# Performance work log

Hardware: AMD Instinct MI355X
Metric: run time of the kernel (lower is better)

The kernel has to match this reference:

```python
import jax, jax.numpy as jnp
import numpy as np

NUM_HEADS = 12
HEAD_SIZE = 64
HIDDEN = NUM_HEADS * HEAD_SIZE  # 768
ONE_SIDED_WINDOW = 256          # attention_window 512 // 2
NEG = -10000.0


def setup_inputs() -> dict:
    key = jax.random.key(0)
    ks = jax.random.split(key, 16)
    B, W, E, H = 1, 2048, 128, HIDDEN
    std = 0.02
    def lin(kw, kb):
        return (jax.random.normal(kw, (H, H), jnp.float32) * std,
                jax.random.normal(kb, (H,), jnp.float32) * std)
    q_w, q_b = lin(ks[0], ks[1])
    k_w, k_b = lin(ks[2], ks[3])
    v_w, v_b = lin(ks[4], ks[5])
    w2e_w, w2e_b = lin(ks[6], ks[7])
    e2w_w, e2w_b = lin(ks[8], ks[9])
    e2e_w, e2e_b = lin(ks[10], ks[11])
    return {
        "word_hidden_states": jax.random.normal(ks[12], (B, W, H), jnp.float32),
        "entity_hidden_states": jax.random.normal(ks[13], (B, E, H), jnp.float32),
        "attention_mask": jnp.zeros((B, 1, 1, W + E), jnp.float32),
        "q_w": q_w, "q_b": q_b, "k_w": k_w, "k_b": k_b, "v_w": v_w, "v_b": v_b,
        "w2e_w": w2e_w, "w2e_b": w2e_b, "e2w_w": e2w_w, "e2w_b": e2w_b,
        "e2e_w": e2e_w, "e2e_b": e2e_b,
    }


def reference(word_hidden_states, entity_hidden_states, attention_mask,
              q_w, q_b, k_w, k_b, v_w, v_b,
              w2e_w, w2e_b, e2w_w, e2w_b, e2e_w, e2e_b):
    B, W, H = word_hidden_states.shape
    E = entity_hidden_states.shape[1]
    S = W + E

    def heads(x):  # [B, L, H] -> [B, nh, L, hd]
        return x.reshape(B, -1, NUM_HEADS, HEAD_SIZE).transpose(0, 2, 1, 3)

    concat = jnp.concatenate([word_hidden_states, entity_hidden_states], axis=1)
    k = heads(concat @ k_w + k_b)          # [B, nh, S, hd]
    v = heads(concat @ v_w + v_b)
    q_w2w = heads(word_hidden_states @ q_w + q_b)
    q_w2e = heads(word_hidden_states @ w2e_w + w2e_b)
    q_e2w = heads(entity_hidden_states @ e2w_w + e2w_b)
    q_e2e = heads(entity_hidden_states @ e2e_w + e2e_b)

    k_word, k_ent = k[:, :, :W], k[:, :, W:]

    # --- w2w: Longformer sliding-window QK^T, then _conversion to a dense
    # [B, nh, W, W] matrix with out-of-band entries set to -10000. ---
    w2w = jnp.einsum('bhid,bhjd->bhij', q_w2w, k_word)  # [B, nh, W, W]
    idx = jnp.arange(W)
    in_band = jnp.abs(idx[:, None] - idx[None, :]) <= ONE_SIDED_WINDOW  # [W, W]
    # diagonal mask: float_mask[j] (-10000 where attention_mask != 0) added
    # within the band (broadcast over heads / query positions)
    mask_words = attention_mask[:, 0, 0, :W]                # [B, W]
    float_mask = jnp.where(mask_words != 0.0, NEG, 0.0)     # [B, W]
    w2w = w2w + float_mask[:, None, None, :]
    # _conversion: out-of-band -> -10000; also exact zeros -> -10000 (source quirk)
    w2w = jnp.where(in_band[None, None] & (w2w != 0.0), w2w, NEG)

    # --- entity-aware dense blocks ---
    w2e = jnp.einsum('bhid,bhjd->bhij', q_w2e, k_ent)    # [B, nh, W, E]
    e2w = jnp.einsum('bhid,bhjd->bhij', q_e2w, k_word)   # [B, nh, E, W]
    e2e = jnp.einsum('bhid,bhjd->bhij', q_e2e, k_ent)    # [B, nh, E, E]

    word_scores = jnp.concatenate([w2w, w2e], axis=3)    # [B, nh, W, S]
    ent_scores = jnp.concatenate([e2w, e2e], axis=3)     # [B, nh, E, S]
    scores = jnp.concatenate([word_scores, ent_scores], axis=2)  # [B, nh, S, S]

    scores = scores / jnp.sqrt(jnp.float32(HEAD_SIZE)) + attention_mask
    probs = jax.nn.softmax(scores, axis=-1)

    ctx = jnp.einsum('bhij,bhjd->bhid', probs, v)        # [B, nh, S, hd]
    ctx = ctx.transpose(0, 2, 1, 3).reshape(B, S, H)
    return ctx[:, :W, :], ctx[:, W:, :]
```

## Files before the change

kernel.cpp:

```cpp
#include <hip/hip_runtime.h>

typedef __bf16 bf16x8 __attribute__((ext_vector_type(8)));
typedef unsigned short u16x8 __attribute__((ext_vector_type(8)));
typedef u16x8 u16x8_a __attribute__((may_alias));
typedef unsigned int u32x4 __attribute__((ext_vector_type(4)));
typedef u32x4 u32x4_a __attribute__((may_alias));
typedef float f32x4 __attribute__((ext_vector_type(4)));

#define LOG2E 1.4426950408889634f
#define NEGV  -10000.0f

__device__ __forceinline__ float bf2f(unsigned short u){
  union{unsigned int i; float f;} x; x.i = ((unsigned int)u)<<16; return x.f;
}
__device__ __forceinline__ unsigned short f2bf(float f){
  union{float f; unsigned int i;} x; x.f=f;
  unsigned int i = x.i;
  return (unsigned short)((i + 0x7FFFu + ((i>>16)&1u)) >> 16);
}
__device__ __forceinline__ u16x8 cvt8(float4 a, float4 b){
  u16x8 r;
  r[0]=f2bf(a.x); r[1]=f2bf(a.y); r[2]=f2bf(a.z); r[3]=f2bf(a.w);
  r[4]=f2bf(b.x); r[5]=f2bf(b.y); r[6]=f2bf(b.z); r[7]=f2bf(b.w);
  return r;
}
__device__ __forceinline__ bf16x8 ldb(const unsigned short* p){
  return __builtin_bit_cast(bf16x8, *(const u16x8_a*)p);
}

__global__ __launch_bounds__(256) void transpose6(
    const float* __restrict__ w0, const float* __restrict__ w1,
    const float* __restrict__ w2, const float* __restrict__ w3,
    const float* __restrict__ w4, const float* __restrict__ w5,
    unsigned short* __restrict__ outT)
{
  const float* src;
  switch (blockIdx.z){
    case 0: src = w0; break; case 1: src = w1; break; case 2: src = w2; break;
    case 3: src = w3; break; case 4: src = w4; break; default: src = w5; break;
  }
  unsigned short* dst = outT + (size_t)blockIdx.z * 589824;
  __shared__ float tile[32][33];
  int tx = threadIdx.x, ty = threadIdx.y;
  int x0 = blockIdx.x*32, y0 = blockIdx.y*32;
  #pragma unroll
  for (int i=0;i<32;i+=8) tile[ty+i][tx] = src[(size_t)(y0+ty+i)*768 + x0+tx];
  __syncthreads();
  #pragma unroll
  for (int i=0;i<32;i+=8) dst[(size_t)(x0+ty+i)*768 + y0+tx] = f2bf(tile[tx][ty+i]);
}

__global__ __launch_bounds__(256) void transpose_v(
    const unsigned short* __restrict__ Vb, unsigned short* __restrict__ VbT)
{
  __shared__ unsigned short t[32][33];
  int tx = threadIdx.x, ty = threadIdx.y;
  int x0 = blockIdx.x*32;
  int y0 = blockIdx.y*32;
  #pragma unroll
  for (int i=0;i<32;i+=8) t[ty+i][tx] = Vb[(size_t)(x0+ty+i)*768 + y0+tx];
  __syncthreads();
  #pragma unroll
  for (int i=0;i<32;i+=8) VbT[(size_t)(y0+ty+i)*2176 + x0+tx] = t[tx][ty+i];
}

__global__ __launch_bounds__(256) void gemm_proj(
    const float* __restrict__ word, const float* __restrict__ ent,
    const unsigned short* __restrict__ wT,
    const float* __restrict__ bK, const float* __restrict__ bV,
    const float* __restrict__ bQ, const float* __restrict__ bWE,
    const float* __restrict__ bEW, const float* __restrict__ bEE,
    unsigned short* __restrict__ oK, unsigned short* __restrict__ oV,
    unsigned short* __restrict__ oQ, unsigned short* __restrict__ oWE,
    unsigned short* __restrict__ oEW, unsigned short* __restrict__ oEE)
{
  int mt = blockIdx.x, ntile = blockIdx.y;
  int g, mg;
  if      (mt < 17){ g=0; mg=mt;    }
  else if (mt < 34){ g=1; mg=mt-17; }
  else if (mt < 50){ g=2; mg=mt-34; }
  else if (mt < 66){ g=3; mg=mt-50; }
  else if (mt < 67){ g=4; mg=0;     }
  else             { g=5; mg=0;     }
  int m0 = mg*128;
  const float* A;
  if (g<=1)      A = (mg<16) ? (word + (size_t)m0*768) : ent;
  else if (g<=3) A = word + (size_t)m0*768;
  else           A = ent;
  const unsigned short* B = wT + (size_t)g*589824;
  const float* bias; unsigned short* out;
  switch (g){
    case 0: bias=bK;  out=oK;  break;
    case 1: bias=bV;  out=oV;  break;
    case 2: bias=bQ;  out=oQ;  break;
    case 3: bias=bWE; out=oWE; break;
    case 4: bias=bEW; out=oEW; break;
    default:bias=bEE; out=oEE; break;
  }
  out += (size_t)m0*768;
  int n0 = ntile*128;

  __shared__ __align__(16) unsigned short a_s[128*32];
  __shared__ __align__(16) unsigned short b_s[128*32];

  int tid  = threadIdx.x;
  int w    = tid>>6, lane = tid&63, quad = lane>>4, lr = lane&15;
  int wm   = (w&1)*64, wn = (w>>1)*64;

  f32x4 acc[4][4];
  #pragma unroll
  for (int i=0;i<4;i++) for (int j=0;j<4;j++) for (int r=0;r<4;r++) acc[i][j][r]=0.f;

  int ar = tid>>1;
  int ak = (tid&1)*16;
  const float* Arow = A + (size_t)ar*768 + ak;
  const unsigned short* Brow = B + (size_t)(n0+ar)*768 + ak;

  for (int k0=0; k0<768; k0+=32){
    float4 af0 = *(const float4*)(Arow + k0);
    float4 af1 = *(const float4*)(Arow + k0 + 4);
    float4 af2 = *(const float4*)(Arow + k0 + 8);
    float4 af3 = *(const float4*)(Arow + k0 + 12);
    u16x8 av0 = cvt8(af0, af1);
    u16x8 av1 = cvt8(af2, af3);
    u16x8 bv0 = *(const u16x8_a*)(Brow + k0);
    u16x8 bv1 = *(const u16x8_a*)(Brow + k0 + 8);
    __syncthreads();
    *(u16x8_a*)(a_s + ar*32 + ak)     = av0;
    *(u16x8_a*)(a_s + ar*32 + ak + 8) = av1;
    *(u16x8_a*)(b_s + ar*32 + ak)     = bv0;
    *(u16x8_a*)(b_s + ar*32 + ak + 8) = bv1;
    __syncthreads();
    bf16x8 af[4], bfr[4];
    #pragma unroll
    for (int i=0;i<4;i++) af[i]  = ldb(a_s + (wm+i*16+lr)*32 + quad*8);
    #pragma unroll
    for (int i=0;i<4;i++) bfr[i] = ldb(b_s + (wn+i*16+lr)*32 + quad*8);
    #pragma unroll
    for (int i=0;i<4;i++)
      #pragma unroll
      for (int j=0;j<4;j++)
        acc[i][j] = __builtin_amdgcn_mfma_f32_16x16x32_bf16(af[i], bfr[j], acc[i][j], 0,0,0);
  }
  #pragma unroll
  for (int j=0;j<4;j++){
    int col = n0 + wn + j*16 + lr;
    float bb = bias[col];
    #pragma unroll
    for (int i=0;i<4;i++){
      int rowb = wm + i*16 + quad*4;
      #pragma unroll
      for (int r=0;r<4;r++)
        out[(size_t)(rowb+r)*768 + col] = f2bf(acc[i][j][r] + bb);
    }
  }
}

__global__ __launch_bounds__(256) void attn_split(
  const unsigned short* __restrict__ Kb,  const unsigned short* __restrict__ VbT,
  const unsigned short* __restrict__ Qw,  const unsigned short* __restrict__ Qwe,
  const unsigned short* __restrict__ Qew, const unsigned short* __restrict__ Qee,
  const float* __restrict__ am,
  float* __restrict__ outw, float* __restrict__ oute)
{
  int bx = blockIdx.x, h = blockIdx.y;
  int tid = threadIdx.x, w = tid>>6, lane = tid&63, quad = lane>>4, lr = lane&15;
  bool isword = bx < 64;
  int qrb, kh, nsplit;
  const unsigned short *Qa, *Qb;
  float* outp;
  if (isword){ qrb = bx*32 + (w>>1)*16; kh = w&1; nsplit = 2; Qa=Qw;  Qb=Qwe; outp=outw; }
  else       { qrb = (bx-64)*16;        kh = w;   nsplit = 4; Qa=Qew; Qb=Qee; outp=oute; }

  __shared__ __align__(16) unsigned int p32[4][16*24];
  __shared__ float mrg[4][64][24];

  const unsigned short* qr = Qa + (size_t)(qrb+lr)*768 + h*64 + quad*8;
  bf16x8 qa0 = ldb(qr), qa1 = ldb(qr + 32);
  qr = Qb + (size_t)(qrb+lr)*768 + h*64 + quad*8;
  bf16x8 qb0 = ldb(qr), qb1 = ldb(qr + 32);

  float m_r[4], l_r[4];
  f32x4 o[4];
  #pragma unroll
  for (int r=0;r<4;r++){ m_r[r] = -1e30f; l_r[r] = 0.f; }
  #pragma unroll
  for (int n2=0;n2<4;n2++) for (int r=0;r<4;r++) o[n2][r] = 0.f;

  int lo, nw;
  if (isword){
    lo = qrb - 256; if (lo < 0) lo = 0; lo &= ~31;
    int hi = qrb + 272; if (hi > 2048) hi = 2048; hi = (hi + 31) & ~31;
    nw = (hi - lo) >> 5;
  } else { lo = 0; nw = 64; }
  int nc = nw + 4;

  for (int c = kh; c < nc; c += nsplit){
    bool entp = c >= nw;
    int j0 = entp ? (2048 + (c-nw)*32) : (lo + c*32);

    const unsigned short* kp = Kb + (size_t)(j0+lr)*768 + h*64 + quad*8;
    bf16x8 k00 = ldb(kp),          k01 = ldb(kp + 32);
    bf16x8 k10 = ldb(kp + 16*768), k11 = ldb(kp + 16*768 + 32);
    const unsigned short* vp = VbT + (size_t)(h*64 + lr)*2176 + j0 + quad*8;
    bf16x8 v0 = ldb(vp), v1 = ldb(vp + 16*2176), v2 = ldb(vp + 32*2176), v3 = ldb(vp + 48*2176);

    bf16x8 qf0 = entp ? qb0 : qa0;
    bf16x8 qf1 = entp ? qb1 : qa1;
    f32x4 s[2];
    {
      f32x4 z0 = {0.f,0.f,0.f,0.f}, z1 = {0.f,0.f,0.f,0.f};
      z0 = __builtin_amdgcn_mfma_f32_16x16x32_bf16(qf0, k00, z0, 0,0,0);
      z0 = __builtin_amdgcn_mfma_f32_16x16x32_bf16(qf1, k01, z0, 0,0,0);
      z1 = __builtin_amdgcn_mfma_f32_16x16x32_bf16(qf0, k10, z1, 0,0,0);
      z1 = __builtin_amdgcn_mfma_f32_16x16x32_bf16(qf1, k11, z1, 0,0,0);
      s[0] = z0; s[1] = z1;
    }

    float sc[2][4];
    bool wband = isword && !entp;
    #pragma unroll
    for (int t=0;t<2;t++){
      int j = j0 + t*16 + lr;
      float amj  = am[j];
      float addl = amj * LOG2E;
      #pragma unroll
      for (int r=0;r<4;r++){
        float sv = s[t][r];
        if (wband){
          sv += (amj != 0.f) ? NEGV : 0.f;
          int i = qrb + quad*4 + r;
          bool ok = ((unsigned)(i - j + 256) <= 512u) && (sv != 0.f);
          sv = ok ? sv : NEGV;
        }
        sc[t][r] = sv * (LOG2E*0.125f) + addl;
      }
    }

    #pragma unroll
    for (int r=0;r<4;r++){
      float mx = fmaxf(sc[0][r], sc[1][r]);
      mx = fmaxf(mx, __shfl_xor(mx, 1));
      mx = fmaxf(mx, __shfl_xor(mx, 2));
      mx = fmaxf(mx, __shfl_xor(mx, 4));
      mx = fmaxf(mx, __shfl_xor(mx, 8));
      float mn = fmaxf(m_r[r], mx);
      float alpha = exp2f(m_r[r] - mn);
      m_r[r] = mn;
      float p0 = exp2f(sc[0][r]-mn), p1 = exp2f(sc[1][r]-mn);
      unsigned short pb0 = f2bf(p0), pb1 = f2bf(p1);
      float rs = bf2f(pb0) + bf2f(pb1);
      rs += __shfl_xor(rs,1); rs += __shfl_xor(rs,2);
      rs += __shfl_xor(rs,4); rs += __shfl_xor(rs,8);
      l_r[r] = l_r[r]*alpha + rs;
      p32[w][(quad*4+r)*24 + lr] = (unsigned int)pb0 | ((unsigned int)pb1 << 16);
      #pragma unroll
      for (int n2=0;n2<4;n2++) o[n2][r] *= alpha;
    }

    const unsigned int* pbp = &p32[w][lr*24 + (quad&1)*8];
    u32x4 ra = *(const u32x4_a*)pbp;
    u32x4 rb = *(const u32x4_a*)(pbp + 4);
    unsigned int pf32[4];
    if (quad < 2){
      pf32[0] = (ra[0]&0xFFFFu) | (ra[1]<<16);
      pf32[1] = (ra[2]&0xFFFFu) | (ra[3]<<16);
      pf32[2] = (rb[0]&0xFFFFu) | (rb[1]<<16);
      pf32[3] = (rb[2]&0xFFFFu) | (rb[3]<<16);
    } else {
      pf32[0] = (ra[0]>>16) | (ra[1]&0xFFFF0000u);
      pf32[1] = (ra[2]>>16) | (ra[3]&0xFFFF0000u);
      pf32[2] = (rb[0]>>16) | (rb[1]&0xFFFF0000u);
      pf32[3] = (rb[2]>>16) | (rb[3]&0xFFFF0000u);
    }
    u32x4 pfv = {pf32[0], pf32[1], pf32[2], pf32[3]};
    bf16x8 pf = __builtin_bit_cast(bf16x8, pfv);

    o[0] = __builtin_amdgcn_mfma_f32_16x16x32_bf16(pf, v0, o[0], 0,0,0);
    o[1] = __builtin_amdgcn_mfma_f32_16x16x32_bf16(pf, v1, o[1], 0,0,0);
    o[2] = __builtin_amdgcn_mfma_f32_16x16x32_bf16(pf, v2, o[2], 0,0,0);
    o[3] = __builtin_amdgcn_mfma_f32_16x16x32_bf16(pf, v3, o[3], 0,0,0);
  }

  {
    float* my = &mrg[w][lane][0];
    #pragma unroll
    for (int r=0;r<4;r++){ my[r] = m_r[r]; my[4+r] = l_r[r]; }
    #pragma unroll
    for (int n2=0;n2<4;n2++)
      #pragma unroll
      for (int r=0;r<4;r++) my[8+n2*4+r] = o[n2][r];
  }
  __syncthreads();
  if (kh == 0){
    for (int p=1; p<nsplit; p++){
      const float* pr = &mrg[w+p][lane][0];
      #pragma unroll
      for (int r=0;r<4;r++){
        float m2 = pr[r], l2 = pr[4+r];
        float M  = fmaxf(m_r[r], m2);
        float e1 = exp2f(m_r[r]-M), e2 = exp2f(m2-M);
        m_r[r] = M;
        l_r[r] = l_r[r]*e1 + l2*e2;
        #pragma unroll
        for (int n2=0;n2<4;n2++)
          o[n2][r] = o[n2][r]*e1 + pr[8+n2*4+r]*e2;
      }
    }
    #pragma unroll
    for (int n2=0;n2<4;n2++)
      #pragma unroll
      for (int r=0;r<4;r++){
        int row = qrb + quad*4 + r;
        outp[(size_t)row*768 + h*64 + n2*16 + lr] = o[n2][r] / l_r[r];
      }
  }
}

extern "C" void kernel_launch(void* const* d_in, const int* in_sizes, int n_in,
                              void* d_out, int out_size, void* d_ws, size_t ws_size,
                              hipStream_t stream) {
  const float* word  = (const float*)d_in[0];
  const float* ent   = (const float*)d_in[1];
  const float* am    = (const float*)d_in[2];
  const float* q_w   = (const float*)d_in[3];
  const float* q_b   = (const float*)d_in[4];
  const float* k_w   = (const float*)d_in[5];
  const float* k_b   = (const float*)d_in[6];
  const float* v_w   = (const float*)d_in[7];
  const float* v_b   = (const float*)d_in[8];
  const float* w2e_w = (const float*)d_in[9];
  const float* w2e_b = (const float*)d_in[10];
  const float* e2w_w = (const float*)d_in[11];
  const float* e2w_b = (const float*)d_in[12];
  const float* e2e_w = (const float*)d_in[13];
  const float* e2e_b = (const float*)d_in[14];

  unsigned short* ws  = (unsigned short*)d_ws;
  unsigned short* wT  = ws;
  unsigned short* Kb  = wT  + (size_t)6*589824;
  unsigned short* Vb  = Kb  + (size_t)2176*768;
  unsigned short* Qw  = Vb  + (size_t)2176*768;
  unsigned short* Qwe = Qw  + (size_t)2048*768;
  unsigned short* Qew = Qwe + (size_t)2048*768;
  unsigned short* Qee = Qew + (size_t)128*768;
  unsigned short* VbT = Qee + (size_t)128*768;

  float* outw = (float*)d_out;
  float* oute = outw + (size_t)2048*768;

  hipLaunchKernelGGL(transpose6, dim3(24,24,6), dim3(32,8), 0, stream,
                     k_w, v_w, q_w, w2e_w, e2w_w, e2e_w, wT);
  hipLaunchKernelGGL(gemm_proj, dim3(68,6), dim3(256), 0, stream,
                     word, ent, wT, k_b, v_b, q_b, w2e_b, e2w_b, e2e_b,
                     Kb, Vb, Qw, Qwe, Qew, Qee);
  hipLaunchKernelGGL(transpose_v, dim3(68,24), dim3(32,8), 0, stream, Vb, VbT);
  hipLaunchKernelGGL(attn_split, dim3(72,12), dim3(256), 0, stream,
                     Kb, VbT, Qw, Qwe, Qew, Qee, am, outw, oute);
}
```

Baseline: 183.4 us.

## Pre-convert activations to bf16, shrink GEMM M-tile, split attention keys four ways

Activations are converted to bf16 once, inside the weight-transpose kernel, so the projection GEMM no longer converts fp32 rows to bf16 on every N-tile. The GEMM M-tile drops from 128 to 64 rows, which doubles the block count. Attention now gives each block 16 query rows, with all four waves splitting that row group's key chunks, which doubles the attention grid. The aim is better occupancy and less redundant conversion, at the cost of an extra workspace buffer, more blocks reloading B tiles, and more cross-wave merge work.

```diff
diff --git a/kernel.cpp b/kernel.cpp
--- a/kernel.cpp
+++ b/kernel.cpp
@@ -3,6 +3,8 @@
 typedef __bf16 bf16x8 __attribute__((ext_vector_type(8)));
 typedef unsigned short u16x8 __attribute__((ext_vector_type(8)));
 typedef u16x8 u16x8_a __attribute__((may_alias));
+typedef unsigned short u16x4 __attribute__((ext_vector_type(4)));
+typedef u16x4 u16x4_a __attribute__((may_alias));
 typedef unsigned int u32x4 __attribute__((ext_vector_type(4)));
 typedef u32x4 u32x4_a __attribute__((may_alias));
 typedef float f32x4 __attribute__((ext_vector_type(4)));
@@ -18,22 +20,29 @@
   unsigned int i = x.i;
   return (unsigned short)((i + 0x7FFFu + ((i>>16)&1u)) >> 16);
 }
-__device__ __forceinline__ u16x8 cvt8(float4 a, float4 b){
-  u16x8 r;
-  r[0]=f2bf(a.x); r[1]=f2bf(a.y); r[2]=f2bf(a.z); r[3]=f2bf(a.w);
-  r[4]=f2bf(b.x); r[5]=f2bf(b.y); r[6]=f2bf(b.z); r[7]=f2bf(b.w);
-  return r;
-}
 __device__ __forceinline__ bf16x8 ldb(const unsigned short* p){
   return __builtin_bit_cast(bf16x8, *(const u16x8_a*)p);
 }
 
-__global__ __launch_bounds__(256) void transpose6(
+__global__ __launch_bounds__(256) void prep(
     const float* __restrict__ w0, const float* __restrict__ w1,
     const float* __restrict__ w2, const float* __restrict__ w3,
     const float* __restrict__ w4, const float* __restrict__ w5,
-    unsigned short* __restrict__ outT)
+    const float* __restrict__ word, const float* __restrict__ ent,
+    unsigned short* __restrict__ outT, unsigned short* __restrict__ Ab)
 {
+  int tx = threadIdx.x, ty = threadIdx.y;
+  if (blockIdx.z == 6){
+    int blk = blockIdx.y*24 + blockIdx.x;
+    int gtid = blk*256 + ty*32 + tx;
+    for (int idx = gtid; idx < 417792; idx += 147456){
+      float4 v = (idx < 393216) ? ((const float4*)word)[idx]
+                                : ((const float4*)ent)[idx - 393216];
+      u16x4 r; r[0]=f2bf(v.x); r[1]=f2bf(v.y); r[2]=f2bf(v.z); r[3]=f2bf(v.w);
+      *(u16x4_a*)(Ab + (size_t)idx*4) = r;
+    }
+    return;
+  }
   const float* src;
   switch (blockIdx.z){
     case 0: src = w0; break; case 1: src = w1; break; case 2: src = w2; break;
@@ -41,7 +50,6 @@
   }
   unsigned short* dst = outT + (size_t)blockIdx.z * 589824;
   __shared__ float tile[32][33];
-  int tx = threadIdx.x, ty = threadIdx.y;
   int x0 = blockIdx.x*32, y0 = blockIdx.y*32;
   #pragma unroll
   for (int i=0;i<32;i+=8) tile[ty+i][tx] = src[(size_t)(y0+ty+i)*768 + x0+tx];
@@ -64,9 +72,8 @@
   for (int i=0;i<32;i+=8) VbT[(size_t)(y0+ty+i)*2176 + x0+tx] = t[tx][ty+i];
 }
 
-__global__ __launch_bounds__(256) void gemm_proj(
-    const float* __restrict__ word, const float* __restrict__ ent,
-    const unsigned short* __restrict__ wT,
+__global__ __launch_bounds__(256) void gemm2(
+    const unsigned short* __restrict__ Ab, const unsigned short* __restrict__ wT,
     const float* __restrict__ bK, const float* __restrict__ bV,
     const float* __restrict__ bQ, const float* __restrict__ bWE,
     const float* __restrict__ bEW, const float* __restrict__ bEE,
@@ -75,69 +82,58 @@
     unsigned short* __restrict__ oEW, unsigned short* __restrict__ oEE)
 {
   int mt = blockIdx.x, ntile = blockIdx.y;
-  int g, mg;
-  if      (mt < 17){ g=0; mg=mt;    }
-  else if (mt < 34){ g=1; mg=mt-17; }
-  else if (mt < 50){ g=2; mg=mt-34; }
-  else if (mt < 66){ g=3; mg=mt-50; }
-  else if (mt < 67){ g=4; mg=0;     }
-  else             { g=5; mg=0;     }
-  int m0 = mg*128;
-  const float* A;
-  if (g<=1)      A = (mg<16) ? (word + (size_t)m0*768) : ent;
-  else if (g<=3) A = word + (size_t)m0*768;
-  else           A = ent;
+  int g, m0, mo;
+  if      (mt < 34){ g=0; mo=mt;      m0=mo*64; }
+  else if (mt < 68){ g=1; mo=mt-34;   m0=mo*64; }
+  else if (mt <100){ g=2; mo=mt-68;   m0=mo*64; }
+  else if (mt <132){ g=3; mo=mt-100;  m0=mo*64; }
+  else if (mt <134){ g=4; mo=mt-132;  m0=2048+mo*64; }
+  else             { g=5; mo=mt-134;  m0=2048+mo*64; }
+  const unsigned short* A = Ab + (size_t)m0*768;
   const unsigned short* B = wT + (size_t)g*589824;
   const float* bias; unsigned short* out;
   switch (g){
-    case 0: bias=bK;  out=oK;  break;
-    case 1: bias=bV;  out=oV;  break;
-    case 2: bias=bQ;  out=oQ;  break;
-    case 3: bias=bWE; out=oWE; break;
-    case 4: bias=bEW; out=oEW; break;
-    default:bias=bEE; out=oEE; break;
-  }
-  out += (size_t)m0*768;
+    case 0: bias=bK;  out=oK  + (size_t)m0*768;    break;
+    case 1: bias=bV;  out=oV  + (size_t)m0*768;    break;
+    case 2: bias=bQ;  out=oQ  + (size_t)m0*768;    break;
+    case 3: bias=bWE; out=oWE + (size_t)m0*768;    break;
+    case 4: bias=bEW; out=oEW + (size_t)(mo*64)*768; break;
+    default:bias=bEE; out=oEE + (size_t)(mo*64)*768; break;
+  }
   int n0 = ntile*128;
 
-  __shared__ __align__(16) unsigned short a_s[128*32];
+  __shared__ __align__(16) unsigned short a_s[64*32];
   __shared__ __align__(16) unsigned short b_s[128*32];
 
   int tid  = threadIdx.x;
   int w    = tid>>6, lane = tid&63, quad = lane>>4, lr = lane&15;
-  int wm   = (w&1)*64, wn = (w>>1)*64;
-
-  f32x4 acc[4][4];
-  #pragma unroll
-  for (int i=0;i<4;i++) for (int j=0;j<4;j++) for (int r=0;r<4;r++) acc[i][j][r]=0.f;
-
-  int ar = tid>>1;
-  int ak = (tid&1)*16;
-  const float* Arow = A + (size_t)ar*768 + ak;
-  const unsigned short* Brow = B + (size_t)(n0+ar)*768 + ak;
+  int wm   = (w&1)*32, wn = (w>>1)*64;
+
+  f32x4 acc[2][4];
+  #pragma unroll
+  for (int i=0;i<2;i++) for (int j=0;j<4;j++) for (int r=0;r<4;r++) acc[i][j][r]=0.f;
+
+  int ar = tid>>2, ak = (tid&3)*8;
+  int br = tid>>1, bk = (tid&1)*16;
+  const unsigned short* Arow = A + (size_t)ar*768 + ak;
+  const unsigned short* Brow = B + (size_t)(n0+br)*768 + bk;
 
   for (int k0=0; k0<768; k0+=32){
-    float4 af0 = *(const float4*)(Arow + k0);
-    float4 af1 = *(const float4*)(Arow + k0 + 4);
-    float4 af2 = *(const float4*)(Arow + k0 + 8);
-    float4 af3 = *(const float4*)(Arow + k0 + 12);
-    u16x8 av0 = cvt8(af0, af1);
-    u16x8 av1 = cvt8(af2, af3);
+    u16x8 av  = *(const u16x8_a*)(Arow + k0);
     u16x8 bv0 = *(const u16x8_a*)(Brow + k0);
     u16x8 bv1 = *(const u16x8_a*)(Brow + k0 + 8);
     __syncthreads();
-    *(u16x8_a*)(a_s + ar*32 + ak)     = av0;
-    *(u16x8_a*)(a_s + ar*32 + ak + 8) = av1;
-    *(u16x8_a*)(b_s + ar*32 + ak)     = bv0;
-    *(u16x8_a*)(b_s + ar*32 + ak + 8) = bv1;
+    *(u16x8_a*)(a_s + ar*32 + ak)      = av;
+    *(u16x8_a*)(b_s + br*32 + bk)      = bv0;
+    *(u16x8_a*)(b_s + br*32 + bk + 8)  = bv1;
     __syncthreads();
-    bf16x8 af[4], bfr[4];
-    #pragma unroll
-    for (int i=0;i<4;i++) af[i]  = ldb(a_s + (wm+i*16+lr)*32 + quad*8);
-    #pragma unroll
-    for (int i=0;i<4;i++) bfr[i] = ldb(b_s + (wn+i*16+lr)*32 + quad*8);
-    #pragma unroll
-    for (int i=0;i<4;i++)
+    bf16x8 af[2], bfr[4];
+    #pragma unroll
+    for (int i=0;i<2;i++) af[i]  = ldb(a_s + (wm+i*16+lr)*32 + quad*8);
+    #pragma unroll
+    for (int j=0;j<4;j++) bfr[j] = ldb(b_s + (wn+j*16+lr)*32 + quad*8);
+    #pragma unroll
+    for (int i=0;i<2;i++)
       #pragma unroll
       for (int j=0;j<4;j++)
         acc[i][j] = __builtin_amdgcn_mfma_f32_16x16x32_bf16(af[i], bfr[j], acc[i][j], 0,0,0);
@@ -147,7 +143,7 @@
     int col = n0 + wn + j*16 + lr;
     float bb = bias[col];
     #pragma unroll
-    for (int i=0;i<4;i++){
+    for (int i=0;i<2;i++){
       int rowb = wm + i*16 + quad*4;
       #pragma unroll
       for (int r=0;r<4;r++)
@@ -156,7 +152,7 @@
   }
 }
 
-__global__ __launch_bounds__(256) void attn_split(
+__global__ __launch_bounds__(256) void attn4(
   const unsigned short* __restrict__ Kb,  const unsigned short* __restrict__ VbT,
   const unsigned short* __restrict__ Qw,  const unsigned short* __restrict__ Qwe,
   const unsigned short* __restrict__ Qew, const unsigned short* __restrict__ Qee,
@@ -165,12 +161,11 @@
 {
   int bx = blockIdx.x, h = blockIdx.y;
   int tid = threadIdx.x, w = tid>>6, lane = tid&63, quad = lane>>4, lr = lane&15;
-  bool isword = bx < 64;
-  int qrb, kh, nsplit;
-  const unsigned short *Qa, *Qb;
-  float* outp;
-  if (isword){ qrb = bx*32 + (w>>1)*16; kh = w&1; nsplit = 2; Qa=Qw;  Qb=Qwe; outp=outw; }
-  else       { qrb = (bx-64)*16;        kh = w;   nsplit = 4; Qa=Qew; Qb=Qee; outp=oute; }
+  bool isword = bx < 128;
+  int qrb = isword ? bx*16 : (bx-128)*16;
+  const unsigned short* Qa = isword ? Qw  : Qew;
+  const unsigned short* Qb = isword ? Qwe : Qee;
+  float* outp = isword ? outw : oute;
 
   __shared__ __align__(16) unsigned int p32[4][16*24];
   __shared__ float mrg[4][64][24];
@@ -190,12 +185,12 @@
   int lo, nw;
   if (isword){
     lo = qrb - 256; if (lo < 0) lo = 0; lo &= ~31;
-    int hi = qrb + 272; if (hi > 2048) hi = 2048; hi = (hi + 31) & ~31;
+    int hi = qrb + 16 + 256; if (hi > 2048) hi = 2048; hi = (hi + 31) & ~31;
     nw = (hi - lo) >> 5;
   } else { lo = 0; nw = 64; }
   int nc = nw + 4;
 
-  for (int c = kh; c < nc; c += nsplit){
+  for (int c = w; c < nc; c += 4){
     bool entp = c >= nw;
     int j0 = entp ? (2048 + (c-nw)*32) : (lo + c*32);
 
@@ -292,9 +287,9 @@
       for (int r=0;r<4;r++) my[8+n2*4+r] = o[n2][r];
   }
   __syncthreads();
-  if (kh == 0){
-    for (int p=1; p<nsplit; p++){
-      const float* pr = &mrg[w+p][lane][0];
+  if (w == 0){
+    for (int p=1; p<4; p++){
+      const float* pr = &mrg[p][lane][0];
       #pragma unroll
       for (int r=0;r<4;r++){
         float m2 = pr[r], l2 = pr[4+r];
@@ -338,7 +333,8 @@
 
   unsigned short* ws  = (unsigned short*)d_ws;
   unsigned short* wT  = ws;
-  unsigned short* Kb  = wT  + (size_t)6*589824;
+  unsigned short* Ab  = wT  + (size_t)6*589824;
+  unsigned short* Kb  = Ab  + (size_t)2176*768;
   unsigned short* Vb  = Kb  + (size_t)2176*768;
   unsigned short* Qw  = Vb  + (size_t)2176*768;
   unsigned short* Qwe = Qw  + (size_t)2048*768;
@@ -349,12 +345,12 @@
   float* outw = (float*)d_out;
   float* oute = outw + (size_t)2048*768;
 
-  hipLaunchKernelGGL(transpose6, dim3(24,24,6), dim3(32,8), 0, stream,
-                     k_w, v_w, q_w, w2e_w, e2w_w, e2e_w, wT);
-  hipLaunchKernelGGL(gemm_proj, dim3(68,6), dim3(256), 0, stream,
-                     word, ent, wT, k_b, v_b, q_b, w2e_b, e2w_b, e2e_b,
+  hipLaunchKernelGGL(prep, dim3(24,24,7), dim3(32,8), 0, stream,
+                     k_w, v_w, q_w, w2e_w, e2w_w, e2e_w, word, ent, wT, Ab);
+  hipLaunchKernelGGL(gemm2, dim3(136,6), dim3(256), 0, stream,
+                     Ab, wT, k_b, v_b, q_b, w2e_b, e2w_b, e2e_b,
                      Kb, Vb, Qw, Qwe, Qew, Qee);
   hipLaunchKernelGGL(transpose_v, dim3(68,24), dim3(32,8), 0, stream, Vb, VbT);
-  hipLaunchKernelGGL(attn_split, dim3(72,12), dim3(256), 0, stream,
+  hipLaunchKernelGGL(attn4, dim3(136,12), dim3(256), 0, stream,
                      Kb, VbT, Qw, Qwe, Qew, Qee, am, outw, oute);
 }
```

Measured after the change: 189.8 us. 3.5% more time.
